# Optimization experiments

Measured on AMD Instinct MI355X. Metric: run time of the kernel, lower is better.

## Reference

```python
import jax, jax.numpy as jnp
import numpy as np

N, E, C, S, G = 20000, 320000, 32, 64, 64
NRAD, HRAD, OUTS, HHEAD, NSH, NL = 8, 64, 16, 64, 9, 2
RCUT = 5.0
LIDX = np.repeat(np.arange(3), [1, 3, 5])  # l index of each of the 9 sh components


def _sph_harm(u):
    # real spherical harmonics up to l=2 on unit vectors, [E,3] -> [E,9]
    x, y, z = u[:, 0], u[:, 1], u[:, 2]
    s3 = jnp.sqrt(jnp.asarray(3.0, u.dtype))
    return jnp.stack([
        jnp.ones_like(x), x, y, z,
        s3 * x * y, s3 * y * z, 0.5 * (3 * z * z - 1.0), s3 * x * z,
        0.5 * s3 * (x * x - y * y)
    ], axis=1)


def _bessel(r):
    # Bessel radial basis with smooth polynomial envelope, [E] -> [E, NRAD]
    n = jnp.arange(1, NRAD + 1, dtype=r.dtype)
    rs = jnp.clip(r, 1e-6, None)[:, None]
    u = jnp.clip(r / RCUT, 0.0, 1.0)
    env = ((1 - u) ** 2 * (1 + 2 * u))[:, None]
    return jnp.sqrt(2.0 / RCUT) * jnp.sin(n * jnp.pi * rs / RCUT) / rs * env


def setup_inputs() -> dict:
    key = jax.random.key(0)
    ks = jax.random.split(key, 16)
    return {
        'vectors': jax.random.normal(ks[0], (E, 3), jnp.float32),
        'node_species': jax.random.randint(ks[1], (N,), 0, S),
        'senders': jax.random.randint(ks[2], (E,), 0, N),
        'receivers': jax.random.randint(ks[3], (E,), 0, N),
        'graph_id': jnp.sort(jax.random.randint(ks[4], (N,), 0, G)),
        'species_embed': jax.random.normal(ks[5], (S, C), jnp.float32) * 0.1,
        'w_r1': jax.random.normal(ks[6], (NRAD, HRAD), jnp.float32) / np.sqrt(NRAD),
        'b_r1': jnp.zeros((HRAD,), jnp.float32),
        'w_r2': jax.random.normal(ks[7], (NL, HRAD, 3 * C), jnp.float32) / np.sqrt(HRAD),
        'w_mix': jax.random.normal(ks[8], (NL, 3, C, C), jnp.float32) / np.sqrt(C),
        'w_sc': jax.random.normal(ks[9], (NL, S, C, C), jnp.float32) / np.sqrt(C),
        'w_readout': jax.random.normal(ks[10], (C, OUTS), jnp.float32) / np.sqrt(C),
        'ln_gamma': jnp.ones((OUTS,), jnp.float32),
        'ln_beta': jnp.zeros((OUTS,), jnp.float32),
        'w_h1': jax.random.normal(ks[11], (OUTS, HHEAD), jnp.float32) / np.sqrt(OUTS),
        'b_h1': jnp.zeros((HHEAD,), jnp.float32),
        'w_h2': jax.random.normal(ks[12], (HHEAD, 1), jnp.float32) / np.sqrt(HHEAD),
        'b_h2': jnp.zeros((1,), jnp.float32),
        'scale': jnp.ones((), jnp.float32),
        'shift': jnp.zeros((), jnp.float32),
    }


def reference(vectors, node_species, senders, receivers, graph_id, species_embed,
              w_r1, b_r1, w_r2, w_mix, w_sc, w_readout, ln_gamma, ln_beta,
              w_h1, b_h1, w_h2, b_h2, scale, shift):
    lidx = jnp.asarray(LIDX)
    # nan-safe edge norms and unit vectors (safe_norm in source)
    r2 = jnp.sum(vectors ** 2, axis=-1)
    r = jnp.where(r2 == 0, 0.0, jnp.sqrt(jnp.where(r2 == 0, 1.0, r2)))
    u = vectors / jnp.where(r == 0, 1.0, r)[:, None]
    sh = _sph_harm(u)                                  # [E,9]
    rad = jax.nn.silu(_bessel(r) @ w_r1 + b_r1)        # [E,HRAD] radial MLP
    h = species_embed[node_species]                    # [N,C] node embedding
    for li in range(NL):
        # per-edge, per-l, per-channel radial weights, expanded to the 9 sh components
        rw = (rad @ w_r2[li]).reshape(E, 3, C)[:, lidx, :]     # [E,9,C]
        # tensor-product message: radial * sender scalars * Y_lm
        msg = sh[:, :, None] * rw * h[senders][:, None, :]     # [E,9,C]
        agg = jax.ops.segment_sum(msg, receivers, num_segments=N)  # [N,9,C]
        # per-irrep (per-l) channel-mixing linear
        mixed = jnp.einsum('nmc,mcd->nmd', agg, w_mix[li][lidx])   # [N,9,C]
        # species-dependent self-connection on the scalar (l=0) channel
        sc = jnp.einsum('nc,ncd->nd', h, w_sc[li][node_species])   # [N,C]
        h = mixed[:, 0, :] + sc + h                                # residual
    readout = h @ w_readout                            # [N,OUTS] (last-block readout)
    mu = jnp.mean(readout, axis=-1, keepdims=True)
    var = jnp.var(readout, axis=-1, keepdims=True)
    nrm = (readout - mu) * jax.lax.rsqrt(var + 1e-6) * ln_gamma + ln_beta
    node_out = (jax.nn.gelu(nrm @ w_h1 + b_h1) @ w_h2 + b_h2)[:, 0]  # [N]
    gsum = jax.ops.segment_sum(node_out, graph_id, num_segments=G)
    cnt = jax.ops.segment_sum(jnp.ones((N,), node_out.dtype), graph_id, num_segments=G)
    gmean = gsum / jnp.clip(cnt, 1.0, None)            # segment-mean node2graph
    return (gmean * scale + shift)[:, None]            # [G,1]
```

## Files before the change

kernel.cpp:

```cpp
#include <hip/hip_runtime.h>
#include <hip/hip_fp16.h>
#include <cstdint>
#include <cmath>

#define NE 320000
#define NN 20000
#define NG 64

typedef __attribute__((ext_vector_type(8))) short s16x8;
typedef __attribute__((ext_vector_type(4))) float f32x4;

static __device__ __forceinline__ unsigned short f32_to_bf16(float x) {
    unsigned int u = __float_as_uint(x);
    u = (u + 0x7fffu + ((u >> 16) & 1u)) >> 16;
    return (unsigned short)u;
}
static __device__ __forceinline__ float bf16_to_f32(unsigned short h) {
    return __uint_as_float(((unsigned int)h) << 16);
}

__global__ __launch_bounds__(256) void setup_kernel(
    const int* __restrict__ spec, const float* __restrict__ emb,
    float* __restrict__ hA,
    const float* __restrict__ w_r2,
    unsigned short* __restrict__ wt_hi, unsigned short* __restrict__ wt_lo,
    int* __restrict__ deg, float* __restrict__ gz)
{
    int t = blockIdx.x * 256 + threadIdx.x;
    if (t < NN * 32) hA[t] = emb[spec[t >> 5] * 32 + (t & 31)];
    if (t < 4096) {
        int c = t >> 6, k = t & 63;
        float v = w_r2[(c >= 32 ? 6144 : 0) + k * 96 + (c & 31)];
        unsigned short hb = f32_to_bf16(v);
        wt_hi[t] = hb;
        wt_lo[t] = f32_to_bf16(v - bf16_to_f32(hb));
    }
    if (t < NN) deg[t] = 0;
    if (t < 128) gz[t] = 0.0f;
}

__global__ __launch_bounds__(256) void count_kernel(
    const int* __restrict__ recv, int* __restrict__ deg)
{
    int e = blockIdx.x * 256 + threadIdx.x;
    atomicAdd(&deg[recv[e]], 1);
}

__global__ __launch_bounds__(1024) void scan_kernel(
    const int* __restrict__ deg,
    int* __restrict__ rowstart, int* __restrict__ cursor)
{
    __shared__ int tsum[1024];
    const int tid = threadIdx.x;
    const int PER = (NN + 1023) / 1024;
    const int base = tid * PER;

    int s = 0;
    for (int i = 0; i < PER; ++i) {
        int idx = base + i;
        if (idx < NN) s += deg[idx];
    }
    tsum[tid] = s;
    __syncthreads();
    for (int off = 1; off < 1024; off <<= 1) {
        int v = (tid >= off) ? tsum[tid - off] : 0;
        __syncthreads();
        tsum[tid] += v;
        __syncthreads();
    }
    int run = tsum[tid] - s;
    for (int i = 0; i < PER; ++i) {
        int idx = base + i;
        if (idx < NN) {
            rowstart[idx] = run;
            cursor[idx] = run;
            run += deg[idx];
        }
    }
    if (tid == 1023) rowstart[NN] = NE;
}

__global__ __launch_bounds__(256) void scatter_kernel(
    const int* __restrict__ recv, const int* __restrict__ snd,
    int* __restrict__ cursor, int* __restrict__ eidp, int* __restrict__ esnd)
{
    int e = blockIdx.x * 256 + threadIdx.x;
    int slot = atomicAdd(&cursor[recv[e]], 1);
    eidp[slot] = e;
    esnd[slot] = snd[e];
}

__global__ __launch_bounds__(256) void edge_gemm_kernel(
    const float* __restrict__ vectors,
    const float* __restrict__ w_r1,
    const float* __restrict__ b_r1,
    const unsigned short* __restrict__ wt_hi,
    const unsigned short* __restrict__ wt_lo,
    const int* __restrict__ eidp,
    __half* __restrict__ rw0_0,
    __half* __restrict__ rw0_1)
{
    __shared__ __attribute__((aligned(16))) short sh_hi[256 * 72];
    __shared__ __attribute__((aligned(16))) short sh_lo[256 * 72];

    const int tid = threadIdx.x;
    const int slot = blockIdx.x * 256 + tid;
    const int e = eidp[slot];

    float x = vectors[3 * e + 0];
    float y = vectors[3 * e + 1];
    float z = vectors[3 * e + 2];
    float r2 = x * x + y * y + z * z;
    float r = (r2 == 0.0f) ? 0.0f : sqrtf(r2);
    float rs = fmaxf(r, 1e-6f);
    float u = fminf(r * 0.2f, 1.0f);
    float env = (1.0f - u) * (1.0f - u) * (1.0f + 2.0f * u);
    float pref = 0.6324555320336759f * env / rs;
    float theta = 0.6283185307179586f * rs;

    float s1 = __sinf(theta), c1 = __cosf(theta);
    float twoc = 2.0f * c1;
    float b[8];
    {
        float sp = 0.0f, s = s1;
#pragma unroll
        for (int n = 0; n < 8; ++n) {
            b[n] = pref * s;
            float nx = twoc * s - sp;
            sp = s; s = nx;
        }
    }

#pragma unroll
    for (int j0 = 0; j0 < 64; j0 += 8) {
        short hibuf[8], lobuf[8];
#pragma unroll
        for (int jj = 0; jj < 8; ++jj) {
            int j = j0 + jj;
            float pre = b_r1[j];
#pragma unroll
            for (int n = 0; n < 8; ++n) pre = fmaf(b[n], w_r1[n * 64 + j], pre);
            float rj = pre * __builtin_amdgcn_rcpf(1.0f + __expf(-pre));
            unsigned short hb = f32_to_bf16(rj);
            float lov = rj - bf16_to_f32(hb);
            hibuf[jj] = (short)hb;
            lobuf[jj] = (short)f32_to_bf16(lov);
        }
        *(s16x8*)&sh_hi[tid * 72 + j0] =
            (s16x8){hibuf[0],hibuf[1],hibuf[2],hibuf[3],hibuf[4],hibuf[5],hibuf[6],hibuf[7]};
        *(s16x8*)&sh_lo[tid * 72 + j0] =
            (s16x8){lobuf[0],lobuf[1],lobuf[2],lobuf[3],lobuf[4],lobuf[5],lobuf[6],lobuf[7]};
    }

    __syncthreads();

    const int wv = tid >> 6;
    const int l = tid & 63;
    const int lrow = l & 15;
    const int lk = l >> 4;

    s16x8 Bhi[4][2], Blo[4][2];
#pragma unroll
    for (int ct = 0; ct < 4; ++ct)
#pragma unroll
        for (int kt = 0; kt < 2; ++kt) {
            int col = ct * 16 + lrow;
            int kof = kt * 32 + lk * 8;
            Bhi[ct][kt] = *(const s16x8*)(wt_hi + col * 64 + kof);
            Blo[ct][kt] = *(const s16x8*)(wt_lo + col * 64 + kof);
        }

    f32x4 acc[4][4];
#pragma unroll
    for (int rt = 0; rt < 4; ++rt)
#pragma unroll
        for (int ct = 0; ct < 4; ++ct) acc[rt][ct] = (f32x4){0.f, 0.f, 0.f, 0.f};

#pragma unroll
    for (int rt = 0; rt < 4; ++rt) {
        int row = wv * 64 + rt * 16 + lrow;
#pragma unroll
        for (int kt = 0; kt < 2; ++kt) {
            s16x8 ahi = *(const s16x8*)&sh_hi[row * 72 + kt * 32 + lk * 8];
            s16x8 alo = *(const s16x8*)&sh_lo[row * 72 + kt * 32 + lk * 8];
#pragma unroll
            for (int ct = 0; ct < 4; ++ct) {
                acc[rt][ct] = __builtin_amdgcn_mfma_f32_16x16x32_bf16(ahi, Bhi[ct][kt], acc[rt][ct], 0, 0, 0);
                acc[rt][ct] = __builtin_amdgcn_mfma_f32_16x16x32_bf16(alo, Bhi[ct][kt], acc[rt][ct], 0, 0, 0);
                acc[rt][ct] = __builtin_amdgcn_mfma_f32_16x16x32_bf16(ahi, Blo[ct][kt], acc[rt][ct], 0, 0, 0);
            }
        }
    }

    __syncthreads();
    __half* stg = (__half*)sh_hi;
#pragma unroll
    for (int rt = 0; rt < 4; ++rt)
#pragma unroll
        for (int ct = 0; ct < 4; ++ct) {
            int col = ct * 16 + lrow;
#pragma unroll
            for (int rr = 0; rr < 4; ++rr) {
                int erow = wv * 64 + rt * 16 + lk * 4 + rr;
                stg[erow * 72 + col] = __float2half_rn(acc[rt][ct][rr]);
            }
        }
    __syncthreads();
    {
        const s16x8* src = (const s16x8*)&sh_hi[tid * 72];
        size_t sb = (size_t)slot * 32;
        s16x8* d0 = (s16x8*)(rw0_0 + sb);
        s16x8* d1 = (s16x8*)(rw0_1 + sb);
        d0[0] = src[0]; d0[1] = src[1]; d0[2] = src[2]; d0[3] = src[3];
        d1[0] = src[4]; d1[1] = src[5]; d1[2] = src[6]; d1[3] = src[7];
    }
}

__device__ __forceinline__ float agg_update_val(
    const __half* __restrict__ rw0h, const float* __restrict__ hin,
    const int* __restrict__ rowstart, const int* __restrict__ esnd,
    const int* __restrict__ spec,
    const float* __restrict__ wmix0, const float* __restrict__ wscl,
    int t, int n, int c, int half)
{
    int s0 = rowstart[n], s1 = rowstart[n + 1];
    float hv = hin[t];

    float p0 = 0.f, p1 = 0.f, p2 = 0.f, p3 = 0.f;
    int k = s0;
    for (; k + 4 <= s1; k += 4) {
        int sA = esnd[k], sB = esnd[k + 1], sC = esnd[k + 2], sD = esnd[k + 3];
        float rA = __half2float(rw0h[(size_t)k * 32 + c]);
        float rB = __half2float(rw0h[(size_t)(k + 1) * 32 + c]);
        float rC = __half2float(rw0h[(size_t)(k + 2) * 32 + c]);
        float rD = __half2float(rw0h[(size_t)(k + 3) * 32 + c]);
        float hA = hin[(size_t)sA * 32 + c];
        float hB = hin[(size_t)sB * 32 + c];
        float hC = hin[(size_t)sC * 32 + c];
        float hD = hin[(size_t)sD * 32 + c];
        p0 = fmaf(rA, hA, p0);
        p1 = fmaf(rB, hB, p1);
        p2 = fmaf(rC, hC, p2);
        p3 = fmaf(rD, hD, p3);
    }
    for (; k < s1; ++k)
        p0 = fmaf(__half2float(rw0h[(size_t)k * 32 + c]),
                  hin[(size_t)esnd[k] * 32 + c], p0);
    float acc = (p0 + p1) + (p2 + p3);

    const float* wsc = wscl + spec[n] * 1024;
    float m0 = 0.f, m1 = 0.f, q0 = 0.f, q1 = 0.f;
#pragma unroll
    for (int cp = 0; cp < 32; cp += 2) {
        float av0 = __shfl(acc, half + cp);
        float hb0 = __shfl(hv, half + cp);
        float av1 = __shfl(acc, half + cp + 1);
        float hb1 = __shfl(hv, half + cp + 1);
        m0 = fmaf(av0, wmix0[cp * 32 + c], m0);
        q0 = fmaf(hb0, wsc[cp * 32 + c], q0);
        m1 = fmaf(av1, wmix0[(cp + 1) * 32 + c], m1);
        q1 = fmaf(hb1, wsc[(cp + 1) * 32 + c], q1);
    }
    return hv + (m0 + m1) + (q0 + q1);
}

__global__ __launch_bounds__(256) void agg_update_kernel(
    const __half* __restrict__ rw0h, const float* __restrict__ hin,
    const int* __restrict__ rowstart, const int* __restrict__ esnd,
    const int* __restrict__ spec,
    const float* __restrict__ wmix0, const float* __restrict__ wscl,
    float* __restrict__ hout)
{
    int t = blockIdx.x * 256 + threadIdx.x;
    int n = t >> 5, c = t & 31;
    int half = (threadIdx.x & 63) & 32;
    hout[t] = agg_update_val(rw0h, hin, rowstart, esnd, spec, wmix0, wscl,
                             t, n, c, half);
}

__global__ __launch_bounds__(256) void agg_readout_kernel(
    const __half* __restrict__ rw0h, const float* __restrict__ hin,
    const int* __restrict__ rowstart, const int* __restrict__ esnd,
    const int* __restrict__ spec,
    const float* __restrict__ wmix0, const float* __restrict__ wscl,
    const int* __restrict__ gid_arr,
    const float* __restrict__ w_ro,
    const float* __restrict__ gamma, const float* __restrict__ beta,
    const float* __restrict__ w_h1, const float* __restrict__ b_h1,
    const float* __restrict__ w_h2, const float* __restrict__ b_h2,
    float* __restrict__ gsum, float* __restrict__ gcnt)
{
    __shared__ int sgid[8];
    __shared__ float sval[8];

    int t = blockIdx.x * 256 + threadIdx.x;
    int n = t >> 5, c = t & 31;
    int half = (threadIdx.x & 63) & 32;

    float outv = agg_update_val(rw0h, hin, rowstart, esnd, spec, wmix0, wscl,
                                t, n, c, half);

    int o = c & 15;
    float r0 = 0.f, r1 = 0.f, r2 = 0.f, r3 = 0.f;
#pragma unroll
    for (int cp = 0; cp < 32; cp += 4) {
        r0 = fmaf(__shfl(outv, half + cp),     w_ro[cp * 16 + o],       r0);
        r1 = fmaf(__shfl(outv, half + cp + 1), w_ro[(cp + 1) * 16 + o], r1);
        r2 = fmaf(__shfl(outv, half + cp + 2), w_ro[(cp + 2) * 16 + o], r2);
        r3 = fmaf(__shfl(outv, half + cp + 3), w_ro[(cp + 3) * 16 + o], r3);
    }
    float ro = (r0 + r1) + (r2 + r3);

    float ssum = ro;
#pragma unroll
    for (int m = 1; m < 16; m <<= 1) ssum += __shfl_xor(ssum, m);
    float mu = ssum * (1.0f / 16.0f);
    float d = ro - mu;
    float vs = d * d;
#pragma unroll
    for (int m = 1; m < 16; m <<= 1) vs += __shfl_xor(vs, m);
    float inv = rsqrtf(vs * (1.0f / 16.0f) + 1e-6f);
    float nrm = d * inv * gamma[o] + beta[o];

    int j1 = c, j2 = c + 32;
    float a1a = b_h1[j1], a1b = 0.f, a2a = b_h1[j2], a2b = 0.f;
#pragma unroll
    for (int oo = 0; oo < 16; oo += 2) {
        float nv0 = __shfl(nrm, half + oo);
        float nv1 = __shfl(nrm, half + oo + 1);
        a1a = fmaf(nv0, w_h1[oo * 64 + j1], a1a);
        a2a = fmaf(nv0, w_h1[oo * 64 + j2], a2a);
        a1b = fmaf(nv1, w_h1[(oo + 1) * 64 + j1], a1b);
        a2b = fmaf(nv1, w_h1[(oo + 1) * 64 + j2], a2b);
    }
    float a1 = a1a + a1b, a2 = a2a + a2b;
    float g1 = a1 * __builtin_amdgcn_rcpf(
        1.0f + __expf(-1.5957691216057308f * (a1 + 0.044715f * a1 * a1 * a1)));
    float g2 = a2 * __builtin_amdgcn_rcpf(
        1.0f + __expf(-1.5957691216057308f * (a2 + 0.044715f * a2 * a2 * a2)));
    float partial = fmaf(g1, w_h2[j1], g2 * w_h2[j2]);
#pragma unroll
    for (int m = 1; m < 32; m <<= 1) partial += __shfl_xor(partial, m);

    if (c == 0) {
        int hw = threadIdx.x >> 5;
        sgid[hw] = gid_arr[n];
        sval[hw] = partial + b_h2[0];
    }
    __syncthreads();
    if (threadIdx.x == 0) {
        int g0 = sgid[0];
        float accv = sval[0];
        float cnt = 1.0f;
        for (int i = 1; i < 8; ++i) {
            if (sgid[i] == g0) { accv += sval[i]; cnt += 1.0f; }
            else {
                atomicAdd(&gsum[g0], accv);
                atomicAdd(&gcnt[g0], cnt);
                g0 = sgid[i]; accv = sval[i]; cnt = 1.0f;
            }
        }
        atomicAdd(&gsum[g0], accv);
        atomicAdd(&gcnt[g0], cnt);
    }
}

__global__ void finalize_kernel(const float* __restrict__ gsum,
                                const float* __restrict__ gcnt,
                                const float* __restrict__ scale,
                                const float* __restrict__ shift,
                                float* __restrict__ out)
{
    int g = threadIdx.x;
    if (g < NG) out[g] = gsum[g] / fmaxf(gcnt[g], 1.0f) * scale[0] + shift[0];
}

extern "C" void kernel_launch(void* const* d_in, const int* in_sizes, int n_in,
                              void* d_out, int out_size, void* d_ws, size_t ws_size,
                              hipStream_t stream)
{
    const float* vectors       = (const float*)d_in[0];
    const int*   node_species  = (const int*)d_in[1];
    const int*   senders       = (const int*)d_in[2];
    const int*   receivers     = (const int*)d_in[3];
    const int*   graph_id      = (const int*)d_in[4];
    const float* species_embed = (const float*)d_in[5];
    const float* w_r1          = (const float*)d_in[6];
    const float* b_r1          = (const float*)d_in[7];
    const float* w_r2          = (const float*)d_in[8];
    const float* w_mix         = (const float*)d_in[9];
    const float* w_sc          = (const float*)d_in[10];
    const float* w_ro          = (const float*)d_in[11];
    const float* ln_gamma      = (const float*)d_in[12];
    const float* ln_beta       = (const float*)d_in[13];
    const float* w_h1          = (const float*)d_in[14];
    const float* b_h1          = (const float*)d_in[15];
    const float* w_h2          = (const float*)d_in[16];
    const float* b_h2          = (const float*)d_in[17];
    const float* scale         = (const float*)d_in[18];
    const float* shift         = (const float*)d_in[19];
    float* out = (float*)d_out;

    __half* rw0_0 = (__half*)d_ws;
    __half* rw0_1 = rw0_0 + (size_t)NE * 32;
    float* hA     = (float*)(rw0_1 + (size_t)NE * 32);
    float* hB     = hA + (size_t)NN * 32;
    float* gsum   = hB + (size_t)NN * 32;
    float* gcnt   = gsum + NG;
    unsigned short* wt_hi = (unsigned short*)(gcnt + NG);
    unsigned short* wt_lo = wt_hi + 4096;
    int* deg      = (int*)(wt_lo + 4096);
    int* rowstart = deg + NN;
    int* cursor   = rowstart + NN + 1;
    int* eidp     = cursor + NN + 1;
    int* esnd     = eidp + NE;

    setup_kernel<<<(NN * 32 + 255) / 256, 256, 0, stream>>>(
        node_species, species_embed, hA, w_r2, wt_hi, wt_lo, deg, gsum);

    count_kernel<<<NE / 256, 256, 0, stream>>>(receivers, deg);

    scan_kernel<<<1, 1024, 0, stream>>>(deg, rowstart, cursor);

    scatter_kernel<<<NE / 256, 256, 0, stream>>>(
        receivers, senders, cursor, eidp, esnd);

    edge_gemm_kernel<<<NE / 256, 256, 0, stream>>>(
        vectors, w_r1, b_r1, wt_hi, wt_lo, eidp, rw0_0, rw0_1);

    agg_update_kernel<<<(NN * 32) / 256, 256, 0, stream>>>(
        rw0_0, hA, rowstart, esnd, node_species, w_mix, w_sc, hB);

    agg_readout_kernel<<<(NN * 32) / 256, 256, 0, stream>>>(
        rw0_1, hB, rowstart, esnd, node_species, w_mix + 3072, w_sc + 65536,
        graph_id, w_ro, ln_gamma, ln_beta, w_h1, b_h1, w_h2, b_h2, gsum, gcnt);

    finalize_kernel<<<1, 64, 0, stream>>>(gsum, gcnt, scale, shift, out);
}
```

Before: 178.9 us.

## Double thread parallelism in edge GEMM and node aggregation kernels

The edge GEMM kernel now handles 128 edges per 256-thread block. The two halves of the block each compute 32 of the 64 radial-MLP hidden units, and each half writes one layer's output. The aggregation kernels assign a full 64-lane wavefront per node instead of 32 lanes. The two halves interleave the incoming edges and combine their sums with cross-half shuffles, and the mixing and readout matvecs are split across lanes. This raises parallelism and latency hiding for the gather-heavy aggregation and the per-edge MLP, at the cost of more blocks, extra shuffles, and redundant scalar work in the duplicated lanes.

```diff
diff --git a/kernel.cpp b/kernel.cpp
--- a/kernel.cpp
+++ b/kernel.cpp
@@ -6,6 +6,7 @@
 #define NE 320000
 #define NN 20000
 #define NG 64
+#define EPB 128
 
 typedef __attribute__((ext_vector_type(8))) short s16x8;
 typedef __attribute__((ext_vector_type(4))) float f32x4;
@@ -100,11 +101,13 @@
     __half* __restrict__ rw0_0,
     __half* __restrict__ rw0_1)
 {
-    __shared__ __attribute__((aligned(16))) short sh_hi[256 * 72];
-    __shared__ __attribute__((aligned(16))) short sh_lo[256 * 72];
+    __shared__ __attribute__((aligned(16))) short sh_hi[EPB * 72];
+    __shared__ __attribute__((aligned(16))) short sh_lo[EPB * 72];
 
     const int tid = threadIdx.x;
-    const int slot = blockIdx.x * 256 + tid;
+    const int ei  = tid & (EPB - 1);
+    const int jh  = tid >> 7;
+    const int slot = blockIdx.x * EPB + ei;
     const int e = eidp[slot];
 
     float x = vectors[3 * e + 0];
@@ -132,11 +135,11 @@
     }
 
 #pragma unroll
-    for (int j0 = 0; j0 < 64; j0 += 8) {
+    for (int j0 = 0; j0 < 32; j0 += 8) {
         short hibuf[8], lobuf[8];
 #pragma unroll
         for (int jj = 0; jj < 8; ++jj) {
-            int j = j0 + jj;
+            int j = jh * 32 + j0 + jj;
             float pre = b_r1[j];
 #pragma unroll
             for (int n = 0; n < 8; ++n) pre = fmaf(b[n], w_r1[n * 64 + j], pre);
@@ -146,9 +149,9 @@
             hibuf[jj] = (short)hb;
             lobuf[jj] = (short)f32_to_bf16(lov);
         }
-        *(s16x8*)&sh_hi[tid * 72 + j0] =
+        *(s16x8*)&sh_hi[ei * 72 + jh * 32 + j0] =
             (s16x8){hibuf[0],hibuf[1],hibuf[2],hibuf[3],hibuf[4],hibuf[5],hibuf[6],hibuf[7]};
-        *(s16x8*)&sh_lo[tid * 72 + j0] =
+        *(s16x8*)&sh_lo[ei * 72 + jh * 32 + j0] =
             (s16x8){lobuf[0],lobuf[1],lobuf[2],lobuf[3],lobuf[4],lobuf[5],lobuf[6],lobuf[7]};
     }
 
@@ -170,15 +173,15 @@
             Blo[ct][kt] = *(const s16x8*)(wt_lo + col * 64 + kof);
         }
 
-    f32x4 acc[4][4];
-#pragma unroll
-    for (int rt = 0; rt < 4; ++rt)
+    f32x4 acc[2][4];
+#pragma unroll
+    for (int rt = 0; rt < 2; ++rt)
 #pragma unroll
         for (int ct = 0; ct < 4; ++ct) acc[rt][ct] = (f32x4){0.f, 0.f, 0.f, 0.f};
 
 #pragma unroll
-    for (int rt = 0; rt < 4; ++rt) {
-        int row = wv * 64 + rt * 16 + lrow;
+    for (int rt = 0; rt < 2; ++rt) {
+        int row = wv * 32 + rt * 16 + lrow;
 #pragma unroll
         for (int kt = 0; kt < 2; ++kt) {
             s16x8 ahi = *(const s16x8*)&sh_hi[row * 72 + kt * 32 + lk * 8];
@@ -195,24 +198,22 @@
     __syncthreads();
     __half* stg = (__half*)sh_hi;
 #pragma unroll
-    for (int rt = 0; rt < 4; ++rt)
+    for (int rt = 0; rt < 2; ++rt)
 #pragma unroll
         for (int ct = 0; ct < 4; ++ct) {
             int col = ct * 16 + lrow;
 #pragma unroll
             for (int rr = 0; rr < 4; ++rr) {
-                int erow = wv * 64 + rt * 16 + lk * 4 + rr;
+                int erow = wv * 32 + rt * 16 + lk * 4 + rr;
                 stg[erow * 72 + col] = __float2half_rn(acc[rt][ct][rr]);
             }
         }
     __syncthreads();
     {
-        const s16x8* src = (const s16x8*)&sh_hi[tid * 72];
-        size_t sb = (size_t)slot * 32;
-        s16x8* d0 = (s16x8*)(rw0_0 + sb);
-        s16x8* d1 = (s16x8*)(rw0_1 + sb);
-        d0[0] = src[0]; d0[1] = src[1]; d0[2] = src[2]; d0[3] = src[3];
-        d1[0] = src[4]; d1[1] = src[5]; d1[2] = src[6]; d1[3] = src[7];
+        const s16x8* src = (const s16x8*)&stg[ei * 72 + jh * 32];
+        __half* dstp = (jh == 0 ? rw0_0 : rw0_1) + (size_t)slot * 32;
+        s16x8* d = (s16x8*)dstp;
+        d[0] = src[0]; d[1] = src[1]; d[2] = src[2]; d[3] = src[3];
     }
 }
 
@@ -221,19 +222,19 @@
     const int* __restrict__ rowstart, const int* __restrict__ esnd,
     const int* __restrict__ spec,
     const float* __restrict__ wmix0, const float* __restrict__ wscl,
-    int t, int n, int c, int half)
+    int n, int c, int kh, int half)
 {
     int s0 = rowstart[n], s1 = rowstart[n + 1];
-    float hv = hin[t];
+    float hv = hin[(size_t)n * 32 + c];
 
     float p0 = 0.f, p1 = 0.f, p2 = 0.f, p3 = 0.f;
-    int k = s0;
-    for (; k + 4 <= s1; k += 4) {
-        int sA = esnd[k], sB = esnd[k + 1], sC = esnd[k + 2], sD = esnd[k + 3];
+    int k = s0 + kh;
+    for (; k + 6 < s1; k += 8) {
+        int sA = esnd[k], sB = esnd[k + 2], sC = esnd[k + 4], sD = esnd[k + 6];
         float rA = __half2float(rw0h[(size_t)k * 32 + c]);
-        float rB = __half2float(rw0h[(size_t)(k + 1) * 32 + c]);
-        float rC = __half2float(rw0h[(size_t)(k + 2) * 32 + c]);
-        float rD = __half2float(rw0h[(size_t)(k + 3) * 32 + c]);
+        float rB = __half2float(rw0h[(size_t)(k + 2) * 32 + c]);
+        float rC = __half2float(rw0h[(size_t)(k + 4) * 32 + c]);
+        float rD = __half2float(rw0h[(size_t)(k + 6) * 32 + c]);
         float hA = hin[(size_t)sA * 32 + c];
         float hB = hin[(size_t)sB * 32 + c];
         float hC = hin[(size_t)sC * 32 + c];
@@ -243,15 +244,17 @@
         p2 = fmaf(rC, hC, p2);
         p3 = fmaf(rD, hD, p3);
     }
-    for (; k < s1; ++k)
+    for (; k < s1; k += 2)
         p0 = fmaf(__half2float(rw0h[(size_t)k * 32 + c]),
                   hin[(size_t)esnd[k] * 32 + c], p0);
     float acc = (p0 + p1) + (p2 + p3);
+    acc += __shfl_xor(acc, 32);
 
     const float* wsc = wscl + spec[n] * 1024;
     float m0 = 0.f, m1 = 0.f, q0 = 0.f, q1 = 0.f;
 #pragma unroll
-    for (int cp = 0; cp < 32; cp += 2) {
+    for (int i = 0; i < 16; i += 2) {
+        int cp = kh * 16 + i;
         float av0 = __shfl(acc, half + cp);
         float hb0 = __shfl(hv, half + cp);
         float av1 = __shfl(acc, half + cp + 1);
@@ -261,7 +264,9 @@
         m1 = fmaf(av1, wmix0[(cp + 1) * 32 + c], m1);
         q1 = fmaf(hb1, wsc[(cp + 1) * 32 + c], q1);
     }
-    return hv + (m0 + m1) + (q0 + q1);
+    float upd = (m0 + m1) + (q0 + q1);
+    upd += __shfl_xor(upd, 32);
+    return hv + upd;
 }
 
 __global__ __launch_bounds__(256) void agg_update_kernel(
@@ -272,10 +277,12 @@
     float* __restrict__ hout)
 {
     int t = blockIdx.x * 256 + threadIdx.x;
-    int n = t >> 5, c = t & 31;
-    int half = (threadIdx.x & 63) & 32;
-    hout[t] = agg_update_val(rw0h, hin, rowstart, esnd, spec, wmix0, wscl,
-                             t, n, c, half);
+    int n = t >> 6;
+    int lane = threadIdx.x & 63;
+    int c = lane & 31, kh = lane >> 5, half = lane & 32;
+    float outv = agg_update_val(rw0h, hin, rowstart, esnd, spec, wmix0, wscl,
+                                n, c, kh, half);
+    if (kh == 0) hout[(size_t)n * 32 + c] = outv;
 }
 
 __global__ __launch_bounds__(256) void agg_readout_kernel(
@@ -290,26 +297,29 @@
     const float* __restrict__ w_h2, const float* __restrict__ b_h2,
     float* __restrict__ gsum, float* __restrict__ gcnt)
 {
-    __shared__ int sgid[8];
-    __shared__ float sval[8];
+    __shared__ int sgid[4];
+    __shared__ float sval[4];
 
     int t = blockIdx.x * 256 + threadIdx.x;
-    int n = t >> 5, c = t & 31;
-    int half = (threadIdx.x & 63) & 32;
+    int n = t >> 6;
+    int lane = threadIdx.x & 63;
+    int c = lane & 31, kh = lane >> 5, half = lane & 32;
 
     float outv = agg_update_val(rw0h, hin, rowstart, esnd, spec, wmix0, wscl,
-                                t, n, c, half);
-
-    int o = c & 15;
-    float r0 = 0.f, r1 = 0.f, r2 = 0.f, r3 = 0.f;
-#pragma unroll
-    for (int cp = 0; cp < 32; cp += 4) {
-        r0 = fmaf(__shfl(outv, half + cp),     w_ro[cp * 16 + o],       r0);
-        r1 = fmaf(__shfl(outv, half + cp + 1), w_ro[(cp + 1) * 16 + o], r1);
-        r2 = fmaf(__shfl(outv, half + cp + 2), w_ro[(cp + 2) * 16 + o], r2);
-        r3 = fmaf(__shfl(outv, half + cp + 3), w_ro[(cp + 3) * 16 + o], r3);
-    }
-    float ro = (r0 + r1) + (r2 + r3);
+                                n, c, kh, half);
+
+    int o = lane & 15;
+    int q4 = lane >> 4;
+    float r0 = 0.f, r1 = 0.f;
+#pragma unroll
+    for (int i = 0; i < 8; i += 2) {
+        int cp = q4 * 8 + i;
+        r0 = fmaf(__shfl(outv, cp),     w_ro[cp * 16 + o],       r0);
+        r1 = fmaf(__shfl(outv, cp + 1), w_ro[(cp + 1) * 16 + o], r1);
+    }
+    float ro = r0 + r1;
+    ro += __shfl_xor(ro, 16);
+    ro += __shfl_xor(ro, 32);
 
     float ssum = ro;
 #pragma unroll
@@ -322,37 +332,31 @@
     float inv = rsqrtf(vs * (1.0f / 16.0f) + 1e-6f);
     float nrm = d * inv * gamma[o] + beta[o];
 
-    int j1 = c, j2 = c + 32;
-    float a1a = b_h1[j1], a1b = 0.f, a2a = b_h1[j2], a2b = 0.f;
+    int j = lane;
+    float a0 = b_h1[j], a1 = 0.f;
 #pragma unroll
     for (int oo = 0; oo < 16; oo += 2) {
-        float nv0 = __shfl(nrm, half + oo);
-        float nv1 = __shfl(nrm, half + oo + 1);
-        a1a = fmaf(nv0, w_h1[oo * 64 + j1], a1a);
-        a2a = fmaf(nv0, w_h1[oo * 64 + j2], a2a);
-        a1b = fmaf(nv1, w_h1[(oo + 1) * 64 + j1], a1b);
-        a2b = fmaf(nv1, w_h1[(oo + 1) * 64 + j2], a2b);
-    }
-    float a1 = a1a + a1b, a2 = a2a + a2b;
-    float g1 = a1 * __builtin_amdgcn_rcpf(
-        1.0f + __expf(-1.5957691216057308f * (a1 + 0.044715f * a1 * a1 * a1)));
-    float g2 = a2 * __builtin_amdgcn_rcpf(
-        1.0f + __expf(-1.5957691216057308f * (a2 + 0.044715f * a2 * a2 * a2)));
-    float partial = fmaf(g1, w_h2[j1], g2 * w_h2[j2]);
-#pragma unroll
-    for (int m = 1; m < 32; m <<= 1) partial += __shfl_xor(partial, m);
-
-    if (c == 0) {
-        int hw = threadIdx.x >> 5;
-        sgid[hw] = gid_arr[n];
-        sval[hw] = partial + b_h2[0];
+        a0 = fmaf(__shfl(nrm, oo),     w_h1[oo * 64 + j],       a0);
+        a1 = fmaf(__shfl(nrm, oo + 1), w_h1[(oo + 1) * 64 + j], a1);
+    }
+    float a = a0 + a1;
+    float g = a * __builtin_amdgcn_rcpf(
+        1.0f + __expf(-1.5957691216057308f * (a + 0.044715f * a * a * a)));
+    float partial = g * w_h2[j];
+#pragma unroll
+    for (int m = 1; m < 64; m <<= 1) partial += __shfl_xor(partial, m);
+
+    if (lane == 0) {
+        int wv = threadIdx.x >> 6;
+        sgid[wv] = gid_arr[n];
+        sval[wv] = partial + b_h2[0];
     }
     __syncthreads();
     if (threadIdx.x == 0) {
         int g0 = sgid[0];
         float accv = sval[0];
         float cnt = 1.0f;
-        for (int i = 1; i < 8; ++i) {
+        for (int i = 1; i < 4; ++i) {
             if (sgid[i] == g0) { accv += sval[i]; cnt += 1.0f; }
             else {
                 atomicAdd(&gsum[g0], accv);
@@ -425,13 +429,13 @@
     scatter_kernel<<<NE / 256, 256, 0, stream>>>(
         receivers, senders, cursor, eidp, esnd);
 
-    edge_gemm_kernel<<<NE / 256, 256, 0, stream>>>(
+    edge_gemm_kernel<<<NE / EPB, 256, 0, stream>>>(
         vectors, w_r1, b_r1, wt_hi, wt_lo, eidp, rw0_0, rw0_1);
 
-    agg_update_kernel<<<(NN * 32) / 256, 256, 0, stream>>>(
+    agg_update_kernel<<<(NN * 64) / 256, 256, 0, stream>>>(
         rw0_0, hA, rowstart, esnd, node_species, w_mix, w_sc, hB);
 
-    agg_readout_kernel<<<(NN * 32) / 256, 256, 0, stream>>>(
+    agg_readout_kernel<<<(NN * 64) / 256, 256, 0, stream>>>(
         rw0_1, hB, rowstart, esnd, node_species, w_mix + 3072, w_sc + 65536,
         graph_id, w_ro, ln_gamma, ln_beta, w_h1, b_h1, w_h2, b_h2, gsum, gcnt);
 
```

Result: slower. 211.9 us (+18.5%).
